# Optimization experiments

Measured on AMD Instinct MI355X. Metric: run time of the kernel, lower is better.

## Reference

```python
import jax, jax.numpy as jnp
import numpy as np

B, C, H, W, K = 16, 512, 64, 64, 7
LN_EPS = 1e-5


def setup_inputs() -> dict:
    key = jax.random.key(0)
    ks = jax.random.split(key, 6)
    x = jax.random.normal(ks[0], (B, C, H, W), dtype=jnp.float32)
    # 1x1 conv C -> K*K (stored as [K*K, C]) + bias
    K_w = jax.random.normal(ks[1], (K * K, C), dtype=jnp.float32) * 0.02
    K_b = jnp.zeros((K * K,), dtype=jnp.float32)
    # 1x1 conv C -> C (conv0)
    conv0_w = jax.random.normal(ks[2], (C, C), dtype=jnp.float32) * 0.02
    conv0_b = jnp.zeros((C,), dtype=jnp.float32)
    # LayerNorm over [C, K, K]
    ln_w = jnp.ones((C, K, K), dtype=jnp.float32)
    ln_b = jnp.zeros((C, K, K), dtype=jnp.float32)
    # 1x1 conv C -> C (conv1)
    conv1_w = jax.random.normal(ks[3], (C, C), dtype=jnp.float32) * 0.02
    conv1_b = jnp.zeros((C,), dtype=jnp.float32)
    return {"x": x, "K_w": K_w, "K_b": K_b, "conv0_w": conv0_w,
            "conv0_b": conv0_b, "ln_w": ln_w, "ln_b": ln_b,
            "conv1_w": conv1_w, "conv1_b": conv1_b}


def reference(x, K_w, K_b, conv0_w, conv0_b, ln_w, ln_b, conv1_w, conv1_b):
    b, c, h, w = x.shape
    kk = K_w.shape[0]          # k*k
    k = int(round(kk ** 0.5))  # kernel size
    hw = h * w

    # query: b c (h w)
    query = x.reshape(b, c, hw)
    # key: 1x1 conv C -> k*k, then b (h w) kk, softmax over (h w)
    key = jnp.einsum('bchw,oc->bohw', x, K_w) + K_b[None, :, None, None]
    key = key.reshape(b, kk, hw).transpose(0, 2, 1)  # [b, hw, kk]
    key = jax.nn.softmax(key, axis=1)                # softmax over spatial dim

    # attention-pooled dynamic filters: [b, c, kk] -> [b, c, k, k]
    filters = jnp.einsum('bcn,bnk->bck', query, key).reshape(b, c, k, k)

    # conv0 (1x1 over channel dim)
    filters = jnp.einsum('bcij,oc->boij', filters, conv0_w) + conv0_b[None, :, None, None]

    # LayerNorm over the last three dims [C, k, k]
    mean = jnp.mean(filters, axis=(1, 2, 3), keepdims=True)
    var = jnp.var(filters, axis=(1, 2, 3), keepdims=True)
    filters = (filters - mean) * jax.lax.rsqrt(var + LN_EPS)
    filters = filters * ln_w[None] + ln_b[None]

    filters = jax.nn.relu(filters)

    # conv1 (1x1)
    filters = jnp.einsum('bcij,oc->boij', filters, conv1_w) + conv1_b[None, :, None, None]

    # per-(batch, channel) grouped conv: groups = b*c, one kxk filter each
    wgt = filters.reshape(b * c, 1, k, k)    # OIHW with I=1
    x_r = x.reshape(1, b * c, h, w)          # NCHW
    pad = k // 2
    out = jax.lax.conv_general_dilated(
        x_r, wgt,
        window_strides=(1, 1),
        padding=[(pad, pad), (pad, pad)],
        feature_group_count=b * c,
        dimension_numbers=('NCHW', 'OIHW', 'NCHW'))
    return out.reshape(b, c, h, w)
```

## Files before the change

### kernel.cpp

```cpp
#include <hip/hip_runtime.h>

#define B 16
#define C 512
#define HW 4096
#define KK 49

#define OFF_KWT    0
#define OFF_C0WT   32768
#define OFF_C1WT   294912
#define OFF_STATS  557056
#define OFF_KEYRAW 558624
#define OFF_FSUM   558624
#define OFF_T0     960032
#define OFF_G      1361440
#define OFF_T1     1762848
#define OFF_KSMT   3769888
#define OFF_KPART  7964192
#define OFF_FPART  7964192

__global__ __launch_bounds__(256) void k0_transpose(
    const float* __restrict__ K_w, const float* __restrict__ c0w,
    const float* __restrict__ c1w, float* __restrict__ kwT,
    float* __restrict__ c0wT, float* __restrict__ c1wT) {
  int i = blockIdx.x * 256 + threadIdx.x;
  if (i < 512 * KK) {
    int cc = i / KK, oo = i % KK;
    kwT[cc * 64 + oo] = K_w[oo * 512 + cc];
  }
  if (i < 512 * 512) {
    int cc = i >> 9, oo = i & 511;
    c0wT[i] = c0w[oo * 512 + cc];
    c1wT[i] = c1w[oo * 512 + cc];
  }
}

__global__ __launch_bounds__(256) void k1_key(
    const float* __restrict__ x, const float* __restrict__ kwT,
    float* __restrict__ kpart) {
  int b = blockIdx.y;
  int cs = blockIdx.z;
  int n = blockIdx.x * 256 + threadIdx.x;
  const float* xp = x + ((size_t)(b * C) + cs * 128) * HW + n;
  float acc[KK];
#pragma unroll
  for (int o = 0; o < KK; o++) acc[o] = 0.f;
  for (int c0 = 0; c0 < 128; c0 += 8) {
    float xv[8];
#pragma unroll
    for (int u = 0; u < 8; u++) xv[u] = xp[(size_t)(c0 + u) * HW];
#pragma unroll
    for (int u = 0; u < 8; u++) {
      const float* kw = kwT + (cs * 128 + c0 + u) * 64;
#pragma unroll
      for (int o = 0; o < KK; o++) acc[o] += xv[u] * kw[o];
    }
  }
#pragma unroll
  for (int o = 0; o < KK; o++)
    kpart[((size_t)(cs * B + b) * KK + o) * HW + n] = acc[o];
}

__global__ __launch_bounds__(256) void k1s_sum(
    const float* __restrict__ kpart, const float* __restrict__ Kb,
    float* __restrict__ keyraw) {
  int i = blockIdx.x * 256 + threadIdx.x;
  const int stride = B * KK * HW / 4;
  float4 s = ((const float4*)kpart)[i];
#pragma unroll
  for (int k = 1; k < 4; k++) {
    float4 v = ((const float4*)kpart)[i + k * stride];
    s.x += v.x; s.y += v.y; s.z += v.z; s.w += v.w;
  }
  int o = (i >> 10) % KK;
  float bb = Kb[o];
  s.x += bb; s.y += bb; s.z += bb; s.w += bb;
  ((float4*)keyraw)[i] = s;
}

__global__ __launch_bounds__(256) void k2a_stats(
    const float* __restrict__ keyraw, float* __restrict__ stats) {
  int row = blockIdx.x;
  const float* p = keyraw + (size_t)row * HW;
  int tid = threadIdx.x;
  float4 v[4];
  float mx = -1e30f;
#pragma unroll
  for (int j = 0; j < 4; j++) {
    v[j] = ((const float4*)p)[tid + j * 256];
    mx = fmaxf(mx, fmaxf(fmaxf(v[j].x, v[j].y), fmaxf(v[j].z, v[j].w)));
  }
  for (int s = 32; s > 0; s >>= 1) mx = fmaxf(mx, __shfl_xor(mx, s));
  __shared__ float red[8];
  int wv = tid >> 6, ln = tid & 63;
  if (ln == 0) red[wv] = mx;
  __syncthreads();
  mx = fmaxf(fmaxf(red[0], red[1]), fmaxf(red[2], red[3]));
  float sm = 0.f;
#pragma unroll
  for (int j = 0; j < 4; j++)
    sm += expf(v[j].x - mx) + expf(v[j].y - mx) + expf(v[j].z - mx) +
          expf(v[j].w - mx);
  for (int s = 32; s > 0; s >>= 1) sm += __shfl_xor(sm, s);
  __syncthreads();
  if (ln == 0) red[4 + wv] = sm;
  __syncthreads();
  if (tid == 0) {
    float s4 = red[4] + red[5] + red[6] + red[7];
    stats[row * 2] = mx;
    stats[row * 2 + 1] = 1.f / s4;
  }
}

__global__ __launch_bounds__(256) void k2b_write(
    const float* __restrict__ keyraw, const float* __restrict__ stats,
    float* __restrict__ ksmT) {
  int b = blockIdx.y;
  int n0 = blockIdx.x * 256;
  int tid = threadIdx.x;
  __shared__ float t[KK][257];
  for (int o = 0; o < KK; o++) {
    float mx = stats[(b * KK + o) * 2];
    float ri = stats[(b * KK + o) * 2 + 1];
    float v = keyraw[(size_t)(b * KK + o) * HW + n0 + tid];
    t[o][tid] = expf(v - mx) * ri;
  }
  __syncthreads();
  for (int i = tid; i < 4096; i += 256) {
    int nl = i >> 4, o4 = (i & 15) * 4;
    float4 w;
    w.x = (o4 < KK) ? t[o4][nl] : 0.f;
    w.y = (o4 + 1 < KK) ? t[o4 + 1][nl] : 0.f;
    w.z = (o4 + 2 < KK) ? t[o4 + 2][nl] : 0.f;
    w.w = (o4 + 3 < KK) ? t[o4 + 3][nl] : 0.f;
    ((float4*)(ksmT + (size_t)(b * HW + n0 + nl) * 64))[i & 15] = w;
  }
}

__global__ __launch_bounds__(256) void k3_filters(
    const float* __restrict__ x, const float* __restrict__ ksmT,
    float* __restrict__ fpart) {
  int ct = blockIdx.x;
  int ks = blockIdx.y;
  int b = blockIdx.z;
  int tid = threadIdx.x;
  int c0 = ct * 256;
  int nbase = ks * 128;
  __shared__ float xT[32][261];
  float acc[KK];
#pragma unroll
  for (int o = 0; o < KK; o++) acc[o] = 0.f;
  for (int n0 = nbase; n0 < nbase + 128; n0 += 32) {
#pragma unroll
    for (int k = 0; k < 8; k++) {
      int i = tid + k * 256;
      int cl = i >> 3, nq = i & 7;
      float4 v = *(const float4*)(x + (size_t)(b * C + c0 + cl) * HW + n0 + nq * 4);
      xT[nq * 4 + 0][cl] = v.x;
      xT[nq * 4 + 1][cl] = v.y;
      xT[nq * 4 + 2][cl] = v.z;
      xT[nq * 4 + 3][cl] = v.w;
    }
    __syncthreads();
#pragma unroll 4
    for (int nn = 0; nn < 32; nn++) {
      float xv = xT[nn][tid];
      const float* kp = ksmT + (size_t)(b * HW + n0 + nn) * 64;
#pragma unroll
      for (int o = 0; o < KK; o++) acc[o] += xv * kp[o];
    }
    __syncthreads();
  }
  float* outp = fpart + ((size_t)(ks * B + b) * C + c0 + tid) * KK;
#pragma unroll
  for (int o = 0; o < KK; o++) outp[o] = acc[o];
}

__global__ __launch_bounds__(256) void k3_sum(
    const float* __restrict__ fpart, float* __restrict__ fsum) {
  int i = blockIdx.x * 256 + threadIdx.x;
  const int stride = B * C * KK / 4;
  float4 s = ((const float4*)fpart)[i];
#pragma unroll
  for (int k = 1; k < 32; k++) {
    float4 v = ((const float4*)fpart)[i + k * stride];
    s.x += v.x; s.y += v.y; s.z += v.z; s.w += v.w;
  }
  ((float4*)fsum)[i] = s;
}

__global__ __launch_bounds__(256) void k4_gemm(
    const float* __restrict__ fin, const float* __restrict__ wT,
    const float* __restrict__ bias, float* __restrict__ outp) {
  int og = blockIdx.x;
  int b = blockIdx.y;
  int tid = threadIdx.x, wv = tid >> 6, ln = tid & 63;
  bool act = ln < KK;
  float acc[16];
#pragma unroll
  for (int k = 0; k < 16; k++) acc[k] = 0.f;
  for (int c = wv * 128; c < wv * 128 + 128; c++) {
    float f = act ? fin[(size_t)(b * C + c) * KK + ln] : 0.f;
    const float* w = wT + (size_t)c * C + og * 16;
#pragma unroll
    for (int k = 0; k < 16; k++) acc[k] += f * w[k];
  }
  __shared__ float red[4][64][17];
#pragma unroll
  for (int k = 0; k < 16; k++) red[wv][ln][k] = acc[k];
  __syncthreads();
  if (wv == 0 && act) {
#pragma unroll
    for (int k = 0; k < 16; k++) {
      float s = red[0][ln][k] + red[1][ln][k] + red[2][ln][k] + red[3][ln][k] +
                bias[og * 16 + k];
      outp[(size_t)(b * C + og * 16 + k) * KK + ln] = s;
    }
  }
}

__global__ __launch_bounds__(256) void k4_ln(
    const float* __restrict__ t0, const float* __restrict__ lnw,
    const float* __restrict__ lnb, float* __restrict__ g) {
  int b = blockIdx.x, tid = threadIdx.x;
  const int NE = C * KK;
  const float* p = t0 + (size_t)b * NE;
  float s = 0.f, q = 0.f;
  for (int i = tid; i < NE / 4; i += 256) {
    float4 v = ((const float4*)p)[i];
    s += v.x + v.y + v.z + v.w;
    q += v.x * v.x + v.y * v.y + v.z * v.z + v.w * v.w;
  }
  for (int sh = 32; sh > 0; sh >>= 1) {
    s += __shfl_xor(s, sh);
    q += __shfl_xor(q, sh);
  }
  __shared__ float rs[4], rq[4];
  int wv = tid >> 6, ln = tid & 63;
  if (ln == 0) { rs[wv] = s; rq[wv] = q; }
  __syncthreads();
  s = rs[0] + rs[1] + rs[2] + rs[3];
  q = rq[0] + rq[1] + rq[2] + rq[3];
  float mean = s / NE;
  float var = q / NE - mean * mean;
  float rstd = rsqrtf(var + 1e-5f);
  float* go = g + (size_t)b * NE;
  for (int i = tid; i < NE; i += 256) {
    float v = (p[i] - mean) * rstd * lnw[i] + lnb[i];
    go[i] = fmaxf(v, 0.f);
  }
}

__global__ __launch_bounds__(256) void k5_dwconv(
    const float* __restrict__ x, const float* __restrict__ filt,
    float* __restrict__ outp) {
  int c = blockIdx.x, b = blockIdx.y, tid = threadIdx.x;
  __shared__ float xs[70][76];
  for (int i = tid; i < 70 * 19; i += 256)
    ((float4*)&xs[0][0])[i] = make_float4(0.f, 0.f, 0.f, 0.f);
  __syncthreads();
  const float* xp = x + (size_t)(b * C + c) * HW;
  for (int i = tid; i < 1024; i += 256) {
    int r = i >> 4, c4 = (i & 15) * 4;
    float4 v = ((const float4*)(xp + r * 64))[i & 15];
    xs[3 + r][3 + c4 + 0] = v.x;
    xs[3 + r][3 + c4 + 1] = v.y;
    xs[3 + r][3 + c4 + 2] = v.z;
    xs[3 + r][3 + c4 + 3] = v.w;
  }
  const float* fp = filt + (size_t)(b * C + c) * KK;
  float f[KK];
#pragma unroll
  for (int k = 0; k < KK; k++) f[k] = fp[k];
  __syncthreads();
  int tr = (tid >> 4) * 4, tc = (tid & 15) * 4;
  float acc[4][4];
#pragma unroll
  for (int r = 0; r < 4; r++)
#pragma unroll
    for (int j = 0; j < 4; j++) acc[r][j] = 0.f;
#pragma unroll
  for (int ii = 0; ii < 10; ii++) {
    float v[12];
#pragma unroll
    for (int q = 0; q < 3; q++) {
      float4 t4 = *(const float4*)&xs[tr + ii][tc + q * 4];
      v[q * 4 + 0] = t4.x; v[q * 4 + 1] = t4.y;
      v[q * 4 + 2] = t4.z; v[q * 4 + 3] = t4.w;
    }
#pragma unroll
    for (int rr = 0; rr < 4; rr++) {
      int kr = ii - rr;
      if (kr >= 0 && kr < 7) {
#pragma unroll
        for (int jj = 0; jj < 4; jj++)
#pragma unroll
          for (int kc = 0; kc < 7; kc++)
            acc[rr][jj] += f[kr * 7 + kc] * v[jj + kc];
      }
    }
  }
  float* op = outp + (size_t)(b * C + c) * HW;
#pragma unroll
  for (int rr = 0; rr < 4; rr++) {
    float4 w = make_float4(acc[rr][0], acc[rr][1], acc[rr][2], acc[rr][3]);
    *(float4*)(op + (tr + rr) * 64 + tc) = w;
  }
}

extern "C" void kernel_launch(void* const* d_in, const int* in_sizes, int n_in,
                              void* d_out, int out_size, void* d_ws,
                              size_t ws_size, hipStream_t stream) {
  const float* x   = (const float*)d_in[0];
  const float* K_w = (const float*)d_in[1];
  const float* K_b = (const float*)d_in[2];
  const float* c0w = (const float*)d_in[3];
  const float* c0b = (const float*)d_in[4];
  const float* lnw = (const float*)d_in[5];
  const float* lnb = (const float*)d_in[6];
  const float* c1w = (const float*)d_in[7];
  const float* c1b = (const float*)d_in[8];
  float* outp = (float*)d_out;
  float* ws = (float*)d_ws;

  float* kwT    = ws + OFF_KWT;
  float* c0wT   = ws + OFF_C0WT;
  float* c1wT   = ws + OFF_C1WT;
  float* stats  = ws + OFF_STATS;
  float* keyraw = ws + OFF_KEYRAW;
  float* fsum   = ws + OFF_FSUM;
  float* t0     = ws + OFF_T0;
  float* g      = ws + OFF_G;
  float* t1     = ws + OFF_T1;
  float* ksmT   = ws + OFF_KSMT;
  float* kpart  = ws + OFF_KPART;
  float* fpart  = ws + OFF_FPART;

  k0_transpose<<<1024, 256, 0, stream>>>(K_w, c0w, c1w, kwT, c0wT, c1wT);
  k1_key<<<dim3(16, 16, 4), 256, 0, stream>>>(x, kwT, kpart);
  k1s_sum<<<3136, 256, 0, stream>>>(kpart, K_b, keyraw);
  k2a_stats<<<B * KK, 256, 0, stream>>>(keyraw, stats);
  k2b_write<<<dim3(16, 16), 256, 0, stream>>>(keyraw, stats, ksmT);
  k3_filters<<<dim3(2, 32, 16), 256, 0, stream>>>(x, ksmT, fpart);
  k3_sum<<<392, 256, 0, stream>>>(fpart, fsum);
  k4_gemm<<<dim3(32, 16), 256, 0, stream>>>(fsum, c0wT, c0b, t0);
  k4_ln<<<16, 256, 0, stream>>>(t0, lnw, lnb, g);
  k4_gemm<<<dim3(32, 16), 256, 0, stream>>>(g, c1wT, c1b, t1);
  k5_dwconv<<<dim3(C, B), 256, 0, stream>>>(x, t1, outp);
}
```

Before: 523.4 us.

## Split key and filter kernels over output halves, fuse key sum into softmax stats

The key projection and the filter pooling kernels now each compute 25 of the 49 outputs per block, with two overlapping halves at offsets 0 and 24, doubling the grid and cutting per-thread accumulators to raise occupancy. Launch bounds request 8 blocks per CU. The key kernel also prefetches the next 8 channels of x into registers. The separate partial-sum kernel is folded into the stats kernel, which removes one launch and one full pass over the key tensor. In exchange, each block re-reads x for both halves and output index 24 is computed and written twice.

```diff
diff --git a/kernel.cpp b/kernel.cpp
--- a/kernel.cpp
+++ b/kernel.cpp
@@ -17,6 +17,7 @@
 #define OFF_KSMT   3769888
 #define OFF_KPART  7964192
 #define OFF_FPART  7964192
+#define KP_SLICE   3211264
 
 __global__ __launch_bounds__(256) void k0_transpose(
     const float* __restrict__ K_w, const float* __restrict__ c0w,
@@ -34,60 +35,62 @@
   }
 }
 
-__global__ __launch_bounds__(256) void k1_key(
+__global__ __launch_bounds__(256, 8) void k1_key(
     const float* __restrict__ x, const float* __restrict__ kwT,
     float* __restrict__ kpart) {
   int b = blockIdx.y;
-  int cs = blockIdx.z;
+  int cs = blockIdx.z >> 1;
+  int ob = (blockIdx.z & 1) * 24;
   int n = blockIdx.x * 256 + threadIdx.x;
   const float* xp = x + ((size_t)(b * C) + cs * 128) * HW + n;
-  float acc[KK];
-#pragma unroll
-  for (int o = 0; o < KK; o++) acc[o] = 0.f;
+  float acc[25];
+#pragma unroll
+  for (int o = 0; o < 25; o++) acc[o] = 0.f;
+  float xc[8], xn[8];
+#pragma unroll
+  for (int u = 0; u < 8; u++) xc[u] = xp[(size_t)u * HW];
   for (int c0 = 0; c0 < 128; c0 += 8) {
-    float xv[8];
-#pragma unroll
-    for (int u = 0; u < 8; u++) xv[u] = xp[(size_t)(c0 + u) * HW];
+    if (c0 + 8 < 128) {
+#pragma unroll
+      for (int u = 0; u < 8; u++) xn[u] = xp[(size_t)(c0 + 8 + u) * HW];
+    }
 #pragma unroll
     for (int u = 0; u < 8; u++) {
-      const float* kw = kwT + (cs * 128 + c0 + u) * 64;
-#pragma unroll
-      for (int o = 0; o < KK; o++) acc[o] += xv[u] * kw[o];
-    }
-  }
-#pragma unroll
-  for (int o = 0; o < KK; o++)
-    kpart[((size_t)(cs * B + b) * KK + o) * HW + n] = acc[o];
-}
-
-__global__ __launch_bounds__(256) void k1s_sum(
+      const float* kw = kwT + (cs * 128 + c0 + u) * 64 + ob;
+#pragma unroll
+      for (int o = 0; o < 25; o++) acc[o] += xc[u] * kw[o];
+    }
+#pragma unroll
+    for (int u = 0; u < 8; u++) xc[u] = xn[u];
+  }
+  float* op = kpart + (((size_t)(cs * B + b) * KK) + ob) * HW + n;
+#pragma unroll
+  for (int o = 0; o < 25; o++) op[(size_t)o * HW] = acc[o];
+}
+
+__global__ __launch_bounds__(256) void k2a_fused(
     const float* __restrict__ kpart, const float* __restrict__ Kb,
-    float* __restrict__ keyraw) {
-  int i = blockIdx.x * 256 + threadIdx.x;
-  const int stride = B * KK * HW / 4;
-  float4 s = ((const float4*)kpart)[i];
-#pragma unroll
-  for (int k = 1; k < 4; k++) {
-    float4 v = ((const float4*)kpart)[i + k * stride];
-    s.x += v.x; s.y += v.y; s.z += v.z; s.w += v.w;
-  }
-  int o = (i >> 10) % KK;
-  float bb = Kb[o];
-  s.x += bb; s.y += bb; s.z += bb; s.w += bb;
-  ((float4*)keyraw)[i] = s;
-}
-
-__global__ __launch_bounds__(256) void k2a_stats(
-    const float* __restrict__ keyraw, float* __restrict__ stats) {
+    float* __restrict__ keyraw, float* __restrict__ stats) {
   int row = blockIdx.x;
-  const float* p = keyraw + (size_t)row * HW;
+  const float* p = kpart + (size_t)row * HW;
+  float* kout = keyraw + (size_t)row * HW;
   int tid = threadIdx.x;
+  float bb = Kb[row % KK];
   float4 v[4];
   float mx = -1e30f;
 #pragma unroll
   for (int j = 0; j < 4; j++) {
-    v[j] = ((const float4*)p)[tid + j * 256];
-    mx = fmaxf(mx, fmaxf(fmaxf(v[j].x, v[j].y), fmaxf(v[j].z, v[j].w)));
+    int idx = tid + j * 256;
+    float4 s = ((const float4*)p)[idx];
+#pragma unroll
+    for (int k = 1; k < 4; k++) {
+      float4 t = ((const float4*)(p + (size_t)k * KP_SLICE))[idx];
+      s.x += t.x; s.y += t.y; s.z += t.z; s.w += t.w;
+    }
+    s.x += bb; s.y += bb; s.z += bb; s.w += bb;
+    ((float4*)kout)[idx] = s;
+    v[j] = s;
+    mx = fmaxf(mx, fmaxf(fmaxf(s.x, s.y), fmaxf(s.z, s.w)));
   }
   for (int s = 32; s > 0; s >>= 1) mx = fmaxf(mx, __shfl_xor(mx, s));
   __shared__ float red[8];
@@ -136,24 +139,25 @@
   }
 }
 
-__global__ __launch_bounds__(256) void k3_filters(
+__global__ __launch_bounds__(256, 8) void k3_filters(
     const float* __restrict__ x, const float* __restrict__ ksmT,
     float* __restrict__ fpart) {
-  int ct = blockIdx.x;
+  int ct = blockIdx.x >> 1;
+  int ob = (blockIdx.x & 1) * 24;
   int ks = blockIdx.y;
   int b = blockIdx.z;
   int tid = threadIdx.x;
   int c0 = ct * 256;
   int nbase = ks * 128;
-  __shared__ float xT[32][261];
-  float acc[KK];
-#pragma unroll
-  for (int o = 0; o < KK; o++) acc[o] = 0.f;
-  for (int n0 = nbase; n0 < nbase + 128; n0 += 32) {
-#pragma unroll
-    for (int k = 0; k < 8; k++) {
+  __shared__ float xT[16][261];
+  float acc[25];
+#pragma unroll
+  for (int o = 0; o < 25; o++) acc[o] = 0.f;
+  for (int n0 = nbase; n0 < nbase + 128; n0 += 16) {
+#pragma unroll
+    for (int k = 0; k < 4; k++) {
       int i = tid + k * 256;
-      int cl = i >> 3, nq = i & 7;
+      int cl = i >> 2, nq = i & 3;
       float4 v = *(const float4*)(x + (size_t)(b * C + c0 + cl) * HW + n0 + nq * 4);
       xT[nq * 4 + 0][cl] = v.x;
       xT[nq * 4 + 1][cl] = v.y;
@@ -161,18 +165,18 @@
       xT[nq * 4 + 3][cl] = v.w;
     }
     __syncthreads();
-#pragma unroll 4
-    for (int nn = 0; nn < 32; nn++) {
+#pragma unroll
+    for (int nn = 0; nn < 16; nn++) {
       float xv = xT[nn][tid];
-      const float* kp = ksmT + (size_t)(b * HW + n0 + nn) * 64;
-#pragma unroll
-      for (int o = 0; o < KK; o++) acc[o] += xv * kp[o];
+      const float* kp = ksmT + (size_t)(b * HW + n0 + nn) * 64 + ob;
+#pragma unroll
+      for (int o = 0; o < 25; o++) acc[o] += xv * kp[o];
     }
     __syncthreads();
   }
-  float* outp = fpart + ((size_t)(ks * B + b) * C + c0 + tid) * KK;
-#pragma unroll
-  for (int o = 0; o < KK; o++) outp[o] = acc[o];
+  float* outp = fpart + ((size_t)(ks * B + b) * C + c0 + tid) * KK + ob;
+#pragma unroll
+  for (int o = 0; o < 25; o++) outp[o] = acc[o];
 }
 
 __global__ __launch_bounds__(256) void k3_sum(
@@ -336,11 +340,10 @@
   float* fpart  = ws + OFF_FPART;
 
   k0_transpose<<<1024, 256, 0, stream>>>(K_w, c0w, c1w, kwT, c0wT, c1wT);
-  k1_key<<<dim3(16, 16, 4), 256, 0, stream>>>(x, kwT, kpart);
-  k1s_sum<<<3136, 256, 0, stream>>>(kpart, K_b, keyraw);
-  k2a_stats<<<B * KK, 256, 0, stream>>>(keyraw, stats);
+  k1_key<<<dim3(16, 16, 8), 256, 0, stream>>>(x, kwT, kpart);
+  k2a_fused<<<B * KK, 256, 0, stream>>>(kpart, K_b, keyraw, stats);
   k2b_write<<<dim3(16, 16), 256, 0, stream>>>(keyraw, stats, ksmT);
-  k3_filters<<<dim3(2, 32, 16), 256, 0, stream>>>(x, ksmT, fpart);
+  k3_filters<<<dim3(4, 32, 16), 256, 0, stream>>>(x, ksmT, fpart);
   k3_sum<<<392, 256, 0, stream>>>(fpart, fsum);
   k4_gemm<<<dim3(32, 16), 256, 0, stream>>>(fsum, c0wT, c0b, t0);
   k4_ln<<<16, 256, 0, stream>>>(t0, lnw, lnb, g);
```

Measured after the change: 584.0 us. +11.6%, slower.
